# Kernel optimization log

Measured on AMD Instinct MI355X. Metric: run time of the kernel, lower is better.

Reference implementation:

```python
import jax, jax.numpy as jnp
import numpy as np

B, S, D, H = 2, 2048, 1024, 16
DH = D // H


def setup_inputs() -> dict:
    key = jax.random.key(0)
    ks = jax.random.split(key, 12)
    s = 1.0 / np.sqrt(D)
    inp = {
        "query": jax.random.normal(ks[0], (B, S, D), jnp.float32),
        "key": jax.random.normal(ks[1], (B, S, D), jnp.float32),
        "value": jax.random.normal(ks[2], (B, S, D), jnp.float32),
        "Wq": jax.random.uniform(ks[3], (D, D), jnp.float32, -s, s),
        "bq": jax.random.uniform(ks[4], (D,), jnp.float32, -s, s),
        "Wk": jax.random.uniform(ks[5], (D, D), jnp.float32, -s, s),
        "bk": jax.random.uniform(ks[6], (D,), jnp.float32, -s, s),
        "Wv": jax.random.uniform(ks[7], (D, D), jnp.float32, -s, s),
        "bv": jax.random.uniform(ks[8], (D,), jnp.float32, -s, s),
        "Wo": jax.random.uniform(ks[9], (D, D), jnp.float32, -s, s),
        "bo": jax.random.uniform(ks[10], (D,), jnp.float32, -s, s),
    }
    return inp


def reference(query, key, value, Wq, bq, Wk, bk, Wv, bv, Wo, bo):
    # q,k,v: [B,S,D] -> [B,H,S,Dh]
    def split_heads(x):
        return x.reshape(B, S, H, DH).transpose(0, 2, 1, 3)

    q = split_heads(query @ Wq.T + bq)
    k = split_heads(key @ Wk.T + bk)
    v = split_heads(value @ Wv.T + bv)
    scale = 1.0 / jnp.sqrt(jnp.float32(DH))
    scores = jnp.einsum("bhqd,bhkd->bhqk", q, k) * scale  # [B,H,S,S]
    attn = jax.nn.softmax(scores, axis=-1)
    # dropout is identity in eval mode
    out = jnp.einsum("bhqk,bhkd->bhqd", attn, v)  # [B,H,S,Dh]
    out = out.transpose(0, 2, 1, 3).reshape(B, S, D)
    out = out @ Wo.T + bo
    return out, attn
```

## Files before the change

### kernel.cpp

```cpp
#include <hip/hip_runtime.h>

#define SS 2048

typedef __attribute__((ext_vector_type(4))) float floatx4;
typedef __attribute__((ext_vector_type(8))) __bf16 bf16x8;
typedef __attribute__((ext_vector_type(8))) unsigned short ushortx8;

__device__ inline unsigned short f2bf(float f) {
  union { float f; unsigned u; } x; x.f = f;
  unsigned r = x.u + 0x7fffu + ((x.u >> 16) & 1u);
  return (unsigned short)(r >> 16);
}

__global__ __launch_bounds__(256) void cvt_bf16(
    const float* __restrict__ q, const float* __restrict__ k,
    const float* __restrict__ v, const float* __restrict__ wq,
    const float* __restrict__ wk, const float* __restrict__ wv,
    const float* __restrict__ wo, unsigned short* __restrict__ dst)
{
  const size_t f = ((size_t)blockIdx.x * 256 + threadIdx.x) * 4;
  const float* src;
  if (f < 4194304) src = q + f;
  else if (f < 8388608) src = k + (f - 4194304);
  else if (f < 12582912) src = v + (f - 8388608);
  else {
    size_t off = f - 12582912;
    unsigned wi = (unsigned)(off >> 20);
    const float* wp = wi == 0 ? wq : wi == 1 ? wk : wi == 2 ? wv : wo;
    src = wp + (off & 1048575);
  }
  float4 x = *(const float4*)src;
  *(ushort4*)&dst[f] = make_ushort4(f2bf(x.x), f2bf(x.y), f2bf(x.z), f2bf(x.w));
}

__device__ __forceinline__ void gemm_body(
    const unsigned short* __restrict__ X, const unsigned short* __restrict__ W,
    const float* __restrict__ bias, void* __restrict__ outp, int mode)
{
  __shared__ unsigned short lA[128][72];
  __shared__ unsigned short lB[128][72];
  const int t = threadIdx.x;
  const int nb = blockIdx.x, mb = blockIdx.y;
  const int lane = t & 63, w = t >> 6;
  const int lr = lane & 15, lq = lane >> 4;
  const int wm = w >> 1, wn = w & 1;

  floatx4 acc[4][4];
  for (int j = 0; j < 4; ++j) {
    float bj = bias[nb * 128 + wn * 64 + j * 16 + lr];
    floatx4 bj4 = {bj, bj, bj, bj};
    for (int i = 0; i < 4; ++i) acc[i][j] = bj4;
  }

  for (int kc = 0; kc < 16; ++kc) {
    for (int i = 0; i < 4; ++i) {
      int idx = t + i * 256;
      int row = idx >> 3, c = idx & 7;
      *(uint4*)&lA[row][c * 8] =
          *(const uint4*)&X[(size_t)(mb * 128 + row) * 1024 + kc * 64 + c * 8];
      *(uint4*)&lB[row][c * 8] =
          *(const uint4*)&W[(size_t)(nb * 128 + row) * 1024 + kc * 64 + c * 8];
    }
    __syncthreads();
    for (int kk = 0; kk < 2; ++kk) {
      bf16x8 aF[4], bF[4];
      for (int i = 0; i < 4; ++i)
        aF[i] = *(const bf16x8*)&lA[wm * 64 + i * 16 + lr][kk * 32 + lq * 8];
      for (int j = 0; j < 4; ++j)
        bF[j] = *(const bf16x8*)&lB[wn * 64 + j * 16 + lr][kk * 32 + lq * 8];
      for (int i = 0; i < 4; ++i)
        for (int j = 0; j < 4; ++j)
          acc[i][j] = __builtin_amdgcn_mfma_f32_16x16x32_bf16(aF[i], bF[j], acc[i][j], 0, 0, 0);
    }
    __syncthreads();
  }

  if (mode == 2) {
    float* O = (float*)outp;
    for (int i = 0; i < 4; ++i) {
      int m0 = mb * 128 + wm * 64 + i * 16 + lq * 4;
      for (int j = 0; j < 4; ++j) {
        int n = nb * 128 + wn * 64 + j * 16 + lr;
        for (int r = 0; r < 4; ++r)
          O[(size_t)(m0 + r) * 1024 + n] = acc[i][j][r];
      }
    }
  } else if (mode == 0) {
    unsigned short* O = (unsigned short*)outp;
    for (int i = 0; i < 4; ++i) {
      int m0 = mb * 128 + wm * 64 + i * 16 + lq * 4;
      for (int j = 0; j < 4; ++j) {
        int n = nb * 128 + wn * 64 + j * 16 + lr;
        int h = n >> 6, dh = n & 63;
        for (int r = 0; r < 4; ++r) {
          int m = m0 + r;
          int b = m >> 11, s = m & 2047;
          O[((size_t)(b * 16 + h) * 2048 + s) * 64 + dh] = f2bf(acc[i][j][r]);
        }
      }
    }
  } else {
    unsigned short* O = (unsigned short*)outp;
    for (int i = 0; i < 4; ++i) {
      int m0 = mb * 128 + wm * 64 + i * 16 + lq * 4;
      int b = m0 >> 11, s0 = m0 & 2047;
      for (int j = 0; j < 4; ++j) {
        int n = nb * 128 + wn * 64 + j * 16 + lr;
        int h = n >> 6, dh = n & 63;
        *(ushort4*)&O[((size_t)(b * 16 + h) * 64 + dh) * 2048 + s0] =
            make_ushort4(f2bf(acc[i][j][0]), f2bf(acc[i][j][1]),
                         f2bf(acc[i][j][2]), f2bf(acc[i][j][3]));
      }
    }
  }
}

__global__ __launch_bounds__(256) void gemm_qkv(
    const unsigned short* __restrict__ base, const float* __restrict__ bq,
    const float* __restrict__ bk, const float* __restrict__ bv,
    unsigned short* __restrict__ q_s, unsigned short* __restrict__ k_s,
    unsigned short* __restrict__ v_t)
{
  const int z = blockIdx.z;
  const unsigned short* X = base + (size_t)z * 4194304;
  const unsigned short* W = base + 12582912 + (size_t)z * 1048576;
  const float* bias = z == 0 ? bq : z == 1 ? bk : bv;
  void* out = z == 0 ? (void*)q_s : z == 1 ? (void*)k_s : (void*)v_t;
  gemm_body(X, W, bias, out, z == 2 ? 1 : 0);
}

__global__ __launch_bounds__(256) void gemm_out(
    const unsigned short* __restrict__ ctxb, const unsigned short* __restrict__ Wob,
    const float* __restrict__ bo, float* __restrict__ out)
{
  gemm_body(ctxb, Wob, bo, (void*)out, 2);
}

__global__ __launch_bounds__(256) void attn_kernel(
    const unsigned short* __restrict__ Q, const unsigned short* __restrict__ K,
    const unsigned short* __restrict__ Vt, float* __restrict__ attn,
    unsigned short* __restrict__ ctxb)
{
  __shared__ float pf[4][16][68];
  const int t = threadIdx.x;
  const int w = t >> 6, lane = t & 63;
  const int lr = lane & 15, lq = lane >> 4;
  const int bid = blockIdx.x;
  const int vb = ((bid & 7) << 7) | (bid >> 3);
  const int gw = vb * 4 + w;
  const int bh = gw >> 7;
  const int q0 = (gw & 127) * 16;
  const int b = bh >> 4, h = bh & 15;

  const unsigned short* qp = Q + (size_t)bh * SS * 64;
  const unsigned short* kp = K + (size_t)bh * SS * 64;
  const unsigned short* vp = Vt + (size_t)bh * 64 * SS;
  float* aout = attn + (size_t)bh * SS * SS;

  bf16x8 qF[2];
  for (int kk = 0; kk < 2; ++kk)
    qF[kk] = *(const bf16x8*)&qp[(size_t)(q0 + lr) * 64 + kk * 32 + lq * 8];

  const floatx4 zf = {0.f, 0.f, 0.f, 0.f};
  float lsum[4] = {0.f, 0.f, 0.f, 0.f};

  for (int kc = 0; kc < 32; ++kc) {
    for (int nt = 0; nt < 4; ++nt) {
      const size_t kbase = (size_t)(kc * 64 + nt * 16 + lr) * 64 + lq * 8;
      bf16x8 kF0 = *(const bf16x8*)&kp[kbase];
      bf16x8 kF1 = *(const bf16x8*)&kp[kbase + 32];
      floatx4 s = __builtin_amdgcn_mfma_f32_16x16x32_bf16(qF[0], kF0, zf, 0, 0, 0);
      s = __builtin_amdgcn_mfma_f32_16x16x32_bf16(qF[1], kF1, s, 0, 0, 0);
      for (int r = 0; r < 4; ++r)
        lsum[r] += __expf(s[r] * 0.125f);
    }
  }
  float rl[4];
  for (int r = 0; r < 4; ++r) {
    float v = lsum[r];
    v += __shfl_xor(v, 1);
    v += __shfl_xor(v, 2);
    v += __shfl_xor(v, 4);
    v += __shfl_xor(v, 8);
    rl[r] = 1.0f / v;
  }

  floatx4 oF[4];
  for (int nt = 0; nt < 4; ++nt) oF[nt] = zf;

  for (int kc = 0; kc < 32; ++kc) {
    for (int nt = 0; nt < 4; ++nt) {
      const size_t kbase = (size_t)(kc * 64 + nt * 16 + lr) * 64 + lq * 8;
      bf16x8 kF0 = *(const bf16x8*)&kp[kbase];
      bf16x8 kF1 = *(const bf16x8*)&kp[kbase + 32];
      floatx4 s = __builtin_amdgcn_mfma_f32_16x16x32_bf16(qF[0], kF0, zf, 0, 0, 0);
      s = __builtin_amdgcn_mfma_f32_16x16x32_bf16(qF[1], kF1, s, 0, 0, 0);
      for (int r = 0; r < 4; ++r)
        pf[w][lq * 4 + r][nt * 16 + lr] = __expf(s[r] * 0.125f) * rl[r];
    }
    {
      const int sc = lane & 15, sr = lane >> 4;
      for (int i = 0; i < 4; ++i) {
        float4 v4 = *(const float4*)&pf[w][sr + i * 4][sc * 4];
        *(float4*)&aout[(size_t)(q0 + sr + i * 4) * 2048 + kc * 64 + sc * 4] = v4;
      }
    }
    for (int kk = 0; kk < 2; ++kk) {
      const float* pr = &pf[w][lr][kk * 32 + lq * 8];
      float4 p0 = *(const float4*)pr;
      float4 p1 = *(const float4*)(pr + 4);
      union { ushortx8 u; bf16x8 b; } ap;
      ap.u[0] = f2bf(p0.x); ap.u[1] = f2bf(p0.y);
      ap.u[2] = f2bf(p0.z); ap.u[3] = f2bf(p0.w);
      ap.u[4] = f2bf(p1.x); ap.u[5] = f2bf(p1.y);
      ap.u[6] = f2bf(p1.z); ap.u[7] = f2bf(p1.w);
      for (int nt = 0; nt < 4; ++nt) {
        bf16x8 vF = *(const bf16x8*)&vp[(size_t)(nt * 16 + lr) * 2048 + kc * 64 + kk * 32 + lq * 8];
        oF[nt] = __builtin_amdgcn_mfma_f32_16x16x32_bf16(ap.b, vF, oF[nt], 0, 0, 0);
      }
    }
  }

  for (int nt = 0; nt < 4; ++nt)
    for (int r = 0; r < 4; ++r) {
      int row = q0 + lq * 4 + r;
      int col = h * 64 + nt * 16 + lr;
      ctxb[(size_t)(b * 2048 + row) * 1024 + col] = f2bf(oF[nt][r]);
    }
}

extern "C" void kernel_launch(void* const* d_in, const int* in_sizes, int n_in,
                              void* d_out, int out_size, void* d_ws, size_t ws_size,
                              hipStream_t stream) {
  (void)in_sizes; (void)n_in; (void)out_size; (void)ws_size;
  const float* query = (const float*)d_in[0];
  const float* key   = (const float*)d_in[1];
  const float* value = (const float*)d_in[2];
  const float* Wq = (const float*)d_in[3];
  const float* bq = (const float*)d_in[4];
  const float* Wk = (const float*)d_in[5];
  const float* bk = (const float*)d_in[6];
  const float* Wv = (const float*)d_in[7];
  const float* bv = (const float*)d_in[8];
  const float* Wo = (const float*)d_in[9];
  const float* bo = (const float*)d_in[10];
  float* outF = (float*)d_out;

  unsigned short* cw  = (unsigned short*)d_ws;
  unsigned short* q_s = cw + 16777216;
  unsigned short* k_s = q_s + 4194304;
  unsigned short* v_t = k_s + 4194304;
  unsigned short* ctxb = v_t + 4194304;

  cvt_bf16<<<dim3(16384), dim3(256), 0, stream>>>(query, key, value, Wq, Wk, Wv, Wo, cw);
  gemm_qkv<<<dim3(8, 32, 3), dim3(256), 0, stream>>>(cw, bq, bk, bv, q_s, k_s, v_t);
  attn_kernel<<<dim3(1024), dim3(256), 0, stream>>>(q_s, k_s, v_t, outF + 4194304, ctxb);
  gemm_out<<<dim3(8, 32), dim3(256), 0, stream>>>(ctxb, cw + 15728640, bo, outF);
}
```

Before: 960.3 us.

## Pipeline K/V register loads in attention and use direct-to-LDS GEMM loads

The attention kernel now double-buffers K fragments in registers and prefetches V fragments ahead of the MFMA work, so global latency is hidden behind compute. It also adds an occupancy hint of 3 blocks per SM. The GEMMs are templated: they load tiles with global_load_lds into an unpadded LDS buffer using a K-step of 32, and the output projection switches to 128x64 tiles to launch more blocks. The extra prefetch registers may limit occupancy, and the unpadded LDS layout may cause bank conflicts.

```diff
diff --git a/kernel.cpp b/kernel.cpp
--- a/kernel.cpp
+++ b/kernel.cpp
@@ -10,6 +10,12 @@
   union { float f; unsigned u; } x; x.f = f;
   unsigned r = x.u + 0x7fffu + ((x.u >> 16) & 1u);
   return (unsigned short)(r >> 16);
+}
+
+__device__ __forceinline__ void gload_lds16(const void* g, void* l) {
+  __builtin_amdgcn_global_load_lds(
+      (const __attribute__((address_space(1))) unsigned int*)g,
+      (__attribute__((address_space(3))) unsigned int*)l, 16, 0, 0);
 }
 
 __global__ __launch_bounds__(256) void cvt_bf16(
@@ -33,64 +39,71 @@
   *(ushort4*)&dst[f] = make_ushort4(f2bf(x.x), f2bf(x.y), f2bf(x.z), f2bf(x.w));
 }
 
-__device__ __forceinline__ void gemm_body(
+template<int BM, int BN, int MODE>
+__device__ __forceinline__ void gemm_core(
+    unsigned short* lds,
     const unsigned short* __restrict__ X, const unsigned short* __restrict__ W,
-    const float* __restrict__ bias, void* __restrict__ outp, int mode)
-{
-  __shared__ unsigned short lA[128][72];
-  __shared__ unsigned short lB[128][72];
+    const float* __restrict__ bias, void* __restrict__ outp)
+{
+  constexpr int MF = BM / 32, NF = BN / 32;
+  constexpr int C = (BM + BN) / 64;
+  unsigned short* lA = lds;
+  unsigned short* lB = lds + BM * 32;
   const int t = threadIdx.x;
   const int nb = blockIdx.x, mb = blockIdx.y;
   const int lane = t & 63, w = t >> 6;
   const int lr = lane & 15, lq = lane >> 4;
   const int wm = w >> 1, wn = w & 1;
 
-  floatx4 acc[4][4];
-  for (int j = 0; j < 4; ++j) {
-    float bj = bias[nb * 128 + wn * 64 + j * 16 + lr];
-    floatx4 bj4 = {bj, bj, bj, bj};
-    for (int i = 0; i < 4; ++i) acc[i][j] = bj4;
-  }
-
-  for (int kc = 0; kc < 16; ++kc) {
-    for (int i = 0; i < 4; ++i) {
-      int idx = t + i * 256;
-      int row = idx >> 3, c = idx & 7;
-      *(uint4*)&lA[row][c * 8] =
-          *(const uint4*)&X[(size_t)(mb * 128 + row) * 1024 + kc * 64 + c * 8];
-      *(uint4*)&lB[row][c * 8] =
-          *(const uint4*)&W[(size_t)(nb * 128 + row) * 1024 + kc * 64 + c * 8];
+  floatx4 acc[MF][NF];
+  for (int j = 0; j < NF; ++j) {
+    float bj = bias[nb * BN + wn * (BN / 2) + j * 16 + lr];
+    floatx4 b4 = {bj, bj, bj, bj};
+    for (int i = 0; i < MF; ++i) acc[i][j] = b4;
+  }
+
+  for (int kc = 0; kc < 32; ++kc) {
+    for (int c = 0; c < C; ++c) {
+      const int idx = c * 256 + t;
+      const unsigned short* src;
+      if (c * 256 < BM * 4) {
+        const int row = idx >> 2, col = idx & 3;
+        src = &X[(size_t)(mb * BM + row) * 1024 + kc * 32 + col * 8];
+      } else {
+        const int i2 = idx - BM * 4;
+        const int row = i2 >> 2, col = i2 & 3;
+        src = &W[(size_t)(nb * BN + row) * 1024 + kc * 32 + col * 8];
+      }
+      gload_lds16(src, &lds[(size_t)idx * 8]);
     }
     __syncthreads();
-    for (int kk = 0; kk < 2; ++kk) {
-      bf16x8 aF[4], bF[4];
-      for (int i = 0; i < 4; ++i)
-        aF[i] = *(const bf16x8*)&lA[wm * 64 + i * 16 + lr][kk * 32 + lq * 8];
-      for (int j = 0; j < 4; ++j)
-        bF[j] = *(const bf16x8*)&lB[wn * 64 + j * 16 + lr][kk * 32 + lq * 8];
-      for (int i = 0; i < 4; ++i)
-        for (int j = 0; j < 4; ++j)
-          acc[i][j] = __builtin_amdgcn_mfma_f32_16x16x32_bf16(aF[i], bF[j], acc[i][j], 0, 0, 0);
-    }
+    bf16x8 aF[MF], bF[NF];
+    for (int i = 0; i < MF; ++i)
+      aF[i] = *(const bf16x8*)&lA[(wm * (BM / 2) + i * 16 + lr) * 32 + lq * 8];
+    for (int j = 0; j < NF; ++j)
+      bF[j] = *(const bf16x8*)&lB[(wn * (BN / 2) + j * 16 + lr) * 32 + lq * 8];
+    for (int i = 0; i < MF; ++i)
+      for (int j = 0; j < NF; ++j)
+        acc[i][j] = __builtin_amdgcn_mfma_f32_16x16x32_bf16(aF[i], bF[j], acc[i][j], 0, 0, 0);
     __syncthreads();
   }
 
-  if (mode == 2) {
+  if (MODE == 2) {
     float* O = (float*)outp;
-    for (int i = 0; i < 4; ++i) {
-      int m0 = mb * 128 + wm * 64 + i * 16 + lq * 4;
-      for (int j = 0; j < 4; ++j) {
-        int n = nb * 128 + wn * 64 + j * 16 + lr;
+    for (int i = 0; i < MF; ++i) {
+      int m0 = mb * BM + wm * (BM / 2) + i * 16 + lq * 4;
+      for (int j = 0; j < NF; ++j) {
+        int n = nb * BN + wn * (BN / 2) + j * 16 + lr;
         for (int r = 0; r < 4; ++r)
           O[(size_t)(m0 + r) * 1024 + n] = acc[i][j][r];
       }
     }
-  } else if (mode == 0) {
+  } else if (MODE == 0) {
     unsigned short* O = (unsigned short*)outp;
-    for (int i = 0; i < 4; ++i) {
-      int m0 = mb * 128 + wm * 64 + i * 16 + lq * 4;
-      for (int j = 0; j < 4; ++j) {
-        int n = nb * 128 + wn * 64 + j * 16 + lr;
+    for (int i = 0; i < MF; ++i) {
+      int m0 = mb * BM + wm * (BM / 2) + i * 16 + lq * 4;
+      for (int j = 0; j < NF; ++j) {
+        int n = nb * BN + wn * (BN / 2) + j * 16 + lr;
         int h = n >> 6, dh = n & 63;
         for (int r = 0; r < 4; ++r) {
           int m = m0 + r;
@@ -101,11 +114,11 @@
     }
   } else {
     unsigned short* O = (unsigned short*)outp;
-    for (int i = 0; i < 4; ++i) {
-      int m0 = mb * 128 + wm * 64 + i * 16 + lq * 4;
+    for (int i = 0; i < MF; ++i) {
+      int m0 = mb * BM + wm * (BM / 2) + i * 16 + lq * 4;
       int b = m0 >> 11, s0 = m0 & 2047;
-      for (int j = 0; j < 4; ++j) {
-        int n = nb * 128 + wn * 64 + j * 16 + lr;
+      for (int j = 0; j < NF; ++j) {
+        int n = nb * BN + wn * (BN / 2) + j * 16 + lr;
         int h = n >> 6, dh = n & 63;
         *(ushort4*)&O[((size_t)(b * 16 + h) * 64 + dh) * 2048 + s0] =
             make_ushort4(f2bf(acc[i][j][0]), f2bf(acc[i][j][1]),
@@ -121,22 +134,24 @@
     unsigned short* __restrict__ q_s, unsigned short* __restrict__ k_s,
     unsigned short* __restrict__ v_t)
 {
+  __shared__ unsigned short lds[(128 + 128) * 32];
   const int z = blockIdx.z;
   const unsigned short* X = base + (size_t)z * 4194304;
   const unsigned short* W = base + 12582912 + (size_t)z * 1048576;
-  const float* bias = z == 0 ? bq : z == 1 ? bk : bv;
-  void* out = z == 0 ? (void*)q_s : z == 1 ? (void*)k_s : (void*)v_t;
-  gemm_body(X, W, bias, out, z == 2 ? 1 : 0);
-}
-
-__global__ __launch_bounds__(256) void gemm_out(
+  if (z == 0)      gemm_core<128, 128, 0>(lds, X, W, bq, q_s);
+  else if (z == 1) gemm_core<128, 128, 0>(lds, X, W, bk, k_s);
+  else             gemm_core<128, 128, 1>(lds, X, W, bv, v_t);
+}
+
+__global__ __launch_bounds__(256) void gemm_out_k(
     const unsigned short* __restrict__ ctxb, const unsigned short* __restrict__ Wob,
     const float* __restrict__ bo, float* __restrict__ out)
 {
-  gemm_body(ctxb, Wob, bo, (void*)out, 2);
-}
-
-__global__ __launch_bounds__(256) void attn_kernel(
+  __shared__ unsigned short lds[(128 + 64) * 32];
+  gemm_core<128, 64, 2>(lds, ctxb, Wob, bo, out);
+}
+
+__global__ __launch_bounds__(256, 3) void attn_kernel(
     const unsigned short* __restrict__ Q, const unsigned short* __restrict__ K,
     const unsigned short* __restrict__ Vt, float* __restrict__ attn,
     unsigned short* __restrict__ ctxb)
@@ -157,23 +172,44 @@
   const unsigned short* vp = Vt + (size_t)bh * 64 * SS;
   float* aout = attn + (size_t)bh * SS * SS;
 
-  bf16x8 qF[2];
-  for (int kk = 0; kk < 2; ++kk)
-    qF[kk] = *(const bf16x8*)&qp[(size_t)(q0 + lr) * 64 + kk * 32 + lq * 8];
+  bf16x8 qF0 = *(const bf16x8*)&qp[(size_t)(q0 + lr) * 64 + lq * 8];
+  bf16x8 qF1 = *(const bf16x8*)&qp[(size_t)(q0 + lr) * 64 + 32 + lq * 8];
 
   const floatx4 zf = {0.f, 0.f, 0.f, 0.f};
+
+#define LOADK(KC, arr) do { \
+    const unsigned short* kb0 = kp + (size_t)((KC) * 64 + lr) * 64 + lq * 8; \
+    arr[0] = *(const bf16x8*)kb0;              arr[1] = *(const bf16x8*)(kb0 + 32); \
+    arr[2] = *(const bf16x8*)(kb0 + 1024);     arr[3] = *(const bf16x8*)(kb0 + 1024 + 32); \
+    arr[4] = *(const bf16x8*)(kb0 + 2048);     arr[5] = *(const bf16x8*)(kb0 + 2048 + 32); \
+    arr[6] = *(const bf16x8*)(kb0 + 3072);     arr[7] = *(const bf16x8*)(kb0 + 3072 + 32); \
+  } while (0)
+
+#define LOADV(KC, arr) do { \
+    const unsigned short* vb0 = vp + (size_t)lr * 2048 + (KC) * 64 + lq * 8; \
+    arr[0] = *(const bf16x8*)vb0;               arr[4] = *(const bf16x8*)(vb0 + 32); \
+    arr[1] = *(const bf16x8*)(vb0 + 16 * 2048); arr[5] = *(const bf16x8*)(vb0 + 16 * 2048 + 32); \
+    arr[2] = *(const bf16x8*)(vb0 + 32 * 2048); arr[6] = *(const bf16x8*)(vb0 + 32 * 2048 + 32); \
+    arr[3] = *(const bf16x8*)(vb0 + 48 * 2048); arr[7] = *(const bf16x8*)(vb0 + 48 * 2048 + 32); \
+  } while (0)
+
+#define QKSUM(arr) do { \
+    for (int nt = 0; nt < 4; ++nt) { \
+      floatx4 s = __builtin_amdgcn_mfma_f32_16x16x32_bf16(qF0, arr[nt * 2], zf, 0, 0, 0); \
+      s = __builtin_amdgcn_mfma_f32_16x16x32_bf16(qF1, arr[nt * 2 + 1], s, 0, 0, 0); \
+      for (int r = 0; r < 4; ++r) lsum[r] += __expf(s[r] * 0.125f); \
+    } \
+  } while (0)
+
+  bf16x8 kA[8], kB[8];
   float lsum[4] = {0.f, 0.f, 0.f, 0.f};
 
-  for (int kc = 0; kc < 32; ++kc) {
-    for (int nt = 0; nt < 4; ++nt) {
-      const size_t kbase = (size_t)(kc * 64 + nt * 16 + lr) * 64 + lq * 8;
-      bf16x8 kF0 = *(const bf16x8*)&kp[kbase];
-      bf16x8 kF1 = *(const bf16x8*)&kp[kbase + 32];
-      floatx4 s = __builtin_amdgcn_mfma_f32_16x16x32_bf16(qF[0], kF0, zf, 0, 0, 0);
-      s = __builtin_amdgcn_mfma_f32_16x16x32_bf16(qF[1], kF1, s, 0, 0, 0);
-      for (int r = 0; r < 4; ++r)
-        lsum[r] += __expf(s[r] * 0.125f);
-    }
+  LOADK(0, kA);
+  for (int kc = 0; kc < 32; kc += 2) {
+    LOADK(kc + 1, kB);
+    QKSUM(kA);
+    if (kc + 2 < 32) LOADK(kc + 2, kA);
+    QKSUM(kB);
   }
   float rl[4];
   for (int r = 0; r < 4; ++r) {
@@ -187,39 +223,43 @@
 
   floatx4 oF[4];
   for (int nt = 0; nt < 4; ++nt) oF[nt] = zf;
-
-  for (int kc = 0; kc < 32; ++kc) {
-    for (int nt = 0; nt < 4; ++nt) {
-      const size_t kbase = (size_t)(kc * 64 + nt * 16 + lr) * 64 + lq * 8;
-      bf16x8 kF0 = *(const bf16x8*)&kp[kbase];
-      bf16x8 kF1 = *(const bf16x8*)&kp[kbase + 32];
-      floatx4 s = __builtin_amdgcn_mfma_f32_16x16x32_bf16(qF[0], kF0, zf, 0, 0, 0);
-      s = __builtin_amdgcn_mfma_f32_16x16x32_bf16(qF[1], kF1, s, 0, 0, 0);
-      for (int r = 0; r < 4; ++r)
-        pf[w][lq * 4 + r][nt * 16 + lr] = __expf(s[r] * 0.125f) * rl[r];
-    }
-    {
-      const int sc = lane & 15, sr = lane >> 4;
-      for (int i = 0; i < 4; ++i) {
-        float4 v4 = *(const float4*)&pf[w][sr + i * 4][sc * 4];
-        *(float4*)&aout[(size_t)(q0 + sr + i * 4) * 2048 + kc * 64 + sc * 4] = v4;
-      }
-    }
-    for (int kk = 0; kk < 2; ++kk) {
-      const float* pr = &pf[w][lr][kk * 32 + lq * 8];
-      float4 p0 = *(const float4*)pr;
-      float4 p1 = *(const float4*)(pr + 4);
-      union { ushortx8 u; bf16x8 b; } ap;
-      ap.u[0] = f2bf(p0.x); ap.u[1] = f2bf(p0.y);
-      ap.u[2] = f2bf(p0.z); ap.u[3] = f2bf(p0.w);
-      ap.u[4] = f2bf(p1.x); ap.u[5] = f2bf(p1.y);
-      ap.u[6] = f2bf(p1.z); ap.u[7] = f2bf(p1.w);
-      for (int nt = 0; nt < 4; ++nt) {
-        bf16x8 vF = *(const bf16x8*)&vp[(size_t)(nt * 16 + lr) * 2048 + kc * 64 + kk * 32 + lq * 8];
-        oF[nt] = __builtin_amdgcn_mfma_f32_16x16x32_bf16(ap.b, vF, oF[nt], 0, 0, 0);
-      }
-    }
-  }
+  bf16x8 vR[8];
+
+#define PB(KC, KCUR, KNEXT, GUARD) do { \
+    LOADV(KC, vR); \
+    for (int nt = 0; nt < 4; ++nt) { \
+      floatx4 s = __builtin_amdgcn_mfma_f32_16x16x32_bf16(qF0, KCUR[nt * 2], zf, 0, 0, 0); \
+      s = __builtin_amdgcn_mfma_f32_16x16x32_bf16(qF1, KCUR[nt * 2 + 1], s, 0, 0, 0); \
+      for (int r = 0; r < 4; ++r) \
+        pf[w][lq * 4 + r][nt * 16 + lr] = __expf(s[r] * 0.125f) * rl[r]; \
+    } \
+    if (GUARD) LOADK((KC) + 1, KNEXT); \
+    { const int sc = lane & 15, sr = lane >> 4; \
+      for (int i = 0; i < 4; ++i) { \
+        float4 v4 = *(const float4*)&pf[w][sr + i * 4][sc * 4]; \
+        *(float4*)&aout[(size_t)(q0 + sr + i * 4) * 2048 + (KC) * 64 + sc * 4] = v4; } } \
+    for (int kk = 0; kk < 2; ++kk) { \
+      const float* pr = &pf[w][lr][kk * 32 + lq * 8]; \
+      float4 p0 = *(const float4*)pr; \
+      float4 p1 = *(const float4*)(pr + 4); \
+      union { ushortx8 u; bf16x8 bb; } ap; \
+      ap.u[0] = f2bf(p0.x); ap.u[1] = f2bf(p0.y); ap.u[2] = f2bf(p0.z); ap.u[3] = f2bf(p0.w); \
+      ap.u[4] = f2bf(p1.x); ap.u[5] = f2bf(p1.y); ap.u[6] = f2bf(p1.z); ap.u[7] = f2bf(p1.w); \
+      for (int nt2 = 0; nt2 < 4; ++nt2) \
+        oF[nt2] = __builtin_amdgcn_mfma_f32_16x16x32_bf16(ap.bb, vR[kk * 4 + nt2], oF[nt2], 0, 0, 0); \
+    } \
+  } while (0)
+
+  LOADK(0, kA);
+  for (int kc = 0; kc < 32; kc += 2) {
+    PB(kc, kA, kB, 1);
+    PB(kc + 1, kB, kA, (kc + 2) < 32);
+  }
+
+#undef LOADK
+#undef LOADV
+#undef QKSUM
+#undef PB
 
   for (int nt = 0; nt < 4; ++nt)
     for (int r = 0; r < 4; ++r) {
@@ -255,5 +295,5 @@
   cvt_bf16<<<dim3(16384), dim3(256), 0, stream>>>(query, key, value, Wq, Wk, Wv, Wo, cw);
   gemm_qkv<<<dim3(8, 32, 3), dim3(256), 0, stream>>>(cw, bq, bk, bv, q_s, k_s, v_t);
   attn_kernel<<<dim3(1024), dim3(256), 0, stream>>>(q_s, k_s, v_t, outF + 4194304, ctxb);
-  gemm_out<<<dim3(8, 32), dim3(256), 0, stream>>>(ctxb, cw + 15728640, bo, outF);
-}
+  gemm_out_k<<<dim3(16, 32), dim3(256), 0, stream>>>(ctxb, cw + 15728640, bo, outF);
+}
```

Result: no change. 948.8 us (-1.2%).
